# Optimization experiments

Hardware: AMD Instinct MI355X
Metric: run time of the kernel (lower is better)

The kernel has to match this reference:

```python
import jax, jax.numpy as jnp
import numpy as np

N_FFT = 512
HOP = N_FFT // 4  # torch.stft default hop_length
TWO_PI = 2.0 * np.pi


def _stft_phase(x):
    """torch.stft(x, n_fft=512, return_complex=True) phase: center reflect-pad,
    rectangular window, onesided rfft. Returns [F, T'] with F = n_fft//2+1."""
    pad = N_FFT // 2
    xp = jnp.pad(x, (pad, pad), mode='reflect')
    n_frames = (xp.shape[0] - N_FFT) // HOP + 1
    idx = (np.arange(n_frames, dtype=np.int32)[:, None] * HOP
           + np.arange(N_FFT, dtype=np.int32)[None, :])
    frames = xp[idx]                      # [T', n_fft]
    spec = jnp.fft.rfft(frames, axis=-1)  # [T', F]
    return jnp.angle(spec).T              # [F, T']


def _anti_wrap(x):
    return jnp.abs(x - jnp.round(x / TWO_PI) * TWO_PI)


def _gd(p):
    # banded matmul with gd_matrix == out[f] = p[f-1] - p[f], out[0] = -p[0]
    return jnp.concatenate([-p[:1], p[:-1] - p[1:]], axis=0)


def _iaf(p):
    # banded matmul with iaf_matrix along time axis
    return jnp.concatenate([-p[:, :1], p[:, :-1] - p[:, 1:]], axis=1)


def setup_inputs() -> dict:
    key = jax.random.key(0)
    k1, k2 = jax.random.split(key)
    T = 4194304  # 2^22 samples (~262 s @ 16 kHz)
    yd = jax.random.normal(k1, (T,), dtype=jnp.float32)
    td = jax.random.normal(k2, (T,), dtype=jnp.float32)
    return {"yd": yd, "td": td}


def reference(yd, td):
    pr = _stft_phase(yd)  # [F, T']
    pg = _stft_phase(td)
    ip_loss = jnp.mean(_anti_wrap(pr - pg))
    gd_loss = jnp.mean(_anti_wrap(_gd(pr) - _gd(pg)))
    iaf_loss = jnp.mean(_anti_wrap(_iaf(pr) - _iaf(pg)))
    return (ip_loss, gd_loss, iaf_loss)
```

## Files before the change

kernel.cpp:

```cpp
#include <hip/hip_runtime.h>
#include <math.h>

#define HOP     128
#define NSLOTS  256
#define FPW     8
#define PI_F    3.14159265358979323846f
#define PI2_F   1.57079632679489661923f
#define K8      0.70710678118654752440f

#define LDS_FENCE() do { __asm__ volatile("" ::: "memory"); \
                         __builtin_amdgcn_wave_barrier(); } while (0)

struct cpx { float x, y; };
__device__ __forceinline__ cpx cadd(cpx a, cpx b){ return {a.x+b.x, a.y+b.y}; }
__device__ __forceinline__ cpx csub(cpx a, cpx b){ return {a.x-b.x, a.y-b.y}; }
__device__ __forceinline__ cpx cmul(cpx a, cpx b){
    return {fmaf(a.x,b.x,-a.y*b.y), fmaf(a.x,b.y, a.y*b.x)};
}
__device__ __forceinline__ cpx cmulc(cpx a, cpx b){
    return {fmaf(a.x,b.x, a.y*b.y), fmaf(a.y,b.x,-a.x*b.y)};
}

__device__ __forceinline__ float abs_angle(float re, float im) {
    float a = fabsf(im), b = fabsf(re);
    float mn = fminf(a, b), mx = fmaxf(a, b);
    float t = __fdividef(mn, fmaxf(mx, 1e-37f));
    float t2 = t * t;
    float p = fmaf(t2, -0.0117212f, 0.05265332f);
    p = fmaf(t2, p, -0.11643287f);
    p = fmaf(t2, p, 0.19354346f);
    p = fmaf(t2, p, -0.33262347f);
    p = fmaf(t2, p, 0.99997726f);
    float r = t * p;
    r = (a > b) ? (PI2_F - r) : r;
    r = (re < 0.f) ? (PI_F - r) : r;
    return r;
}

__device__ __forceinline__ void dft8(cpx v[8]) {
    cpx a0=cadd(v[0],v[4]), a1=cadd(v[1],v[5]), a2=cadd(v[2],v[6]), a3=cadd(v[3],v[7]);
    cpx b0=csub(v[0],v[4]), b1=csub(v[1],v[5]), b2=csub(v[2],v[6]), b3=csub(v[3],v[7]);
    b1 = cpx{K8*(b1.x+b1.y), K8*(b1.y-b1.x)};
    b2 = cpx{b2.y, -b2.x};
    b3 = cpx{K8*(b3.y-b3.x), -K8*(b3.x+b3.y)};
    cpx c0=cadd(a0,a2), c2=csub(a0,a2);
    cpx c1=cadd(a1,a3), c3=csub(a1,a3); c3 = cpx{c3.y, -c3.x};
    cpx d0=cadd(b0,b2), d2=csub(b0,b2);
    cpx d1=cadd(b1,b3), d3=csub(b1,b3); d3 = cpx{d3.y, -d3.x};
    v[0]=cadd(c0,c1); v[4]=csub(c0,c1);
    v[2]=cadd(c2,c3); v[6]=csub(c2,c3);
    v[1]=cadd(d0,d1); v[5]=csub(d0,d1);
    v[3]=cadd(d2,d3); v[7]=csub(d2,d3);
}

__global__ __launch_bounds__(256, 2) void phase_loss_kernel(
        const float* __restrict__ y, const float* __restrict__ g,
        float* __restrict__ acc, int* __restrict__ ticket,
        float* __restrict__ out, int T, int n_frames, float inv_count) {
    __shared__ float2 xch_all[4][512];
    __shared__ float2 tw2_tab[7][8];
    __shared__ float wsum[3][4];
    __shared__ int is_last;

    const int tid  = threadIdx.x;
    const int lane = tid & 63;
    const int wid  = tid >> 6;
    const int l8   = lane & 7;
    float2* xch = xch_all[wid];

    if (tid < 56) {
        const int k = (tid >> 3) + 1, l = tid & 7;
        float s, c;
        __sincosf(-(2.0f * PI_F / 64.0f) * (float)(l * k), &s, &c);
        tw2_tab[tid >> 3][l] = make_float2(c, s);
    }
    __syncthreads();

    cpx tw1[7];
    #pragma unroll
    for (int k = 1; k < 8; ++k) {
        float a1 = -(2.0f * PI_F / 512.0f) * (float)(lane * k);
        __sincosf(a1, &tw1[k - 1].y, &tw1[k - 1].x);
    }

    float ip = 0.f, gd = 0.f, iaf = 0.f;
    cpx Cp[5];
    const int tmax_int = (T - 256) / HOP;
    const int ra1 = (lane >> 3) * 72 + (lane & 7);
    const int ra2 = (lane >> 3) * 65 + (lane & 7) * 8;
    const int rsl = (lane + 63) & 63;
    const int rsh = (64 - lane) & 63;

    auto load_frame = [&](int t, cpx* vv) {
        const int base = t * HOP - 256 + lane;
        if (t >= 2 && t <= tmax_int) {
            #pragma unroll
            for (int r = 0; r < 8; ++r) {
                int j = base + r * 64;
                vv[r].x = y[j]; vv[r].y = g[j];
            }
        } else {
            #pragma unroll
            for (int r = 0; r < 8; ++r) {
                int j = base + r * 64;
                j = (j < 0) ? -j : j;
                j = (j >= T) ? (2 * T - 2 - j) : j;
                vv[r].x = y[j]; vv[r].y = g[j];
            }
        }
    };

    auto process = [&](cpx* v, bool accum, bool hp) {
        dft8(v);
        #pragma unroll
        for (int k = 1; k < 8; ++k) v[k] = cmul(v[k], tw1[k - 1]);
        LDS_FENCE();
        #pragma unroll
        for (int k = 0; k < 8; ++k)
            xch[lane ^ (72 * k)] = make_float2(v[k].x, v[k].y);
        LDS_FENCE();
        #pragma unroll
        for (int r = 0; r < 8; ++r) {
            float2 tmp = xch[ra1 ^ (r << 3)];
            v[r] = cpx{tmp.x, tmp.y};
        }
        dft8(v);
        #pragma unroll
        for (int k = 1; k < 8; ++k) {
            float2 tw = tw2_tab[k - 1][l8];
            v[k] = cmul(v[k], cpx{tw.x, tw.y});
        }
        LDS_FENCE();
        #pragma unroll
        for (int k = 0; k < 8; ++k)
            xch[lane ^ (65 * k)] = make_float2(v[k].x, v[k].y);
        LDS_FENCE();
        #pragma unroll
        for (int r = 0; r < 8; ++r) {
            float2 tmp = xch[ra2 ^ r];
            v[r] = cpx{tmp.x, tmp.y};
        }
        dft8(v);
        cpx Cc[5];
        #pragma unroll
        for (int jj = 0; jj < 5; ++jj) {
            float px = __shfl(v[7 - jj].x, rsh, 64);
            float py = __shfl(v[7 - jj].y, rsh, 64);
            px = (lane == 0) ? v[(8 - jj) & 7].x : px;
            py = (lane == 0) ? v[(8 - jj) & 7].y : py;
            float ur = v[jj].x + px, ui = v[jj].y - py;
            float vx = v[jj].x - px, vy = v[jj].y + py;
            Cc[jj].x = fmaf(ur, vy, -ui * vx);
            Cc[jj].y = fmaf(ur, vx,  ui * vy);
        }
        if (accum) {
            cpx rprev = {0.f, 0.f};
            #pragma unroll
            for (int jj = 0; jj < 4; ++jj) {
                cpx rj;
                rj.x = __shfl(Cc[jj].x, rsl, 64);
                rj.y = __shfl(Cc[jj].y, rsl, 64);
                cpx cmj = (jj > 0 && lane == 0) ? rprev : rj;
                cpx cc = Cc[jj];
                float aw = abs_angle(cc.x, cc.y);
                ip += aw;
                cpx qg = cmulc(cmj, cc);
                float gt = abs_angle(qg.x, qg.y);
                gd += (jj == 0 && lane == 0) ? aw : gt;
                if (hp) {
                    cpx qi = cmulc(Cp[jj], cc);
                    iaf += abs_angle(qi.x, qi.y);
                } else {
                    iaf += aw;
                }
                rprev = rj;
            }
            if (lane == 0) {
                cpx cc = Cc[4];
                float aw = abs_angle(cc.x, cc.y);
                ip += aw;
                cpx qg = cmulc(rprev, cc);
                gd += abs_angle(qg.x, qg.y);
                if (hp) {
                    cpx qi = cmulc(Cp[4], cc);
                    iaf += abs_angle(qi.x, qi.y);
                } else {
                    iaf += aw;
                }
            }
        }
        #pragma unroll
        for (int jj = 0; jj < 5; ++jj) Cp[jj] = Cc[jj];
    };

    const int chain   = (blockIdx.x << 2) | wid;
    const int nchains = (int)(gridDim.x << 2);
    const int t0 = chain * FPW;
    int tend = t0 + FPW;
    if (chain == nchains - 1) tend = n_frames;
    const bool havep = (t0 > 0);

    cpx v[8];
    if (havep) {
        cpx vp[8];
        load_frame(t0 - 1, vp);
        load_frame(t0, v);
        process(vp, false, false);
    } else {
        load_frame(t0, v);
    }
    #pragma unroll 2
    for (int t = t0; t < tend; ++t) {
        cpx vn[8];
        const bool pf = (t + 1 < tend);
        if (pf) load_frame(t + 1, vn);
        process(v, true, havep || (t > t0));
        if (pf) {
            #pragma unroll
            for (int r = 0; r < 8; ++r) v[r] = vn[r];
        }
    }

    __syncthreads();
    for (int off = 32; off; off >>= 1) {
        ip  += __shfl_down(ip, off);
        gd  += __shfl_down(gd, off);
        iaf += __shfl_down(iaf, off);
    }
    if (lane == 0) { wsum[0][wid] = ip; wsum[1][wid] = gd; wsum[2][wid] = iaf; }
    __syncthreads();
    if (tid == 0) {
        const int slot = (int)(blockIdx.x & (NSLOTS - 1));
        atomicAdd(acc + 0 * NSLOTS + slot, wsum[0][0] + wsum[0][1] + wsum[0][2] + wsum[0][3]);
        atomicAdd(acc + 1 * NSLOTS + slot, wsum[1][0] + wsum[1][1] + wsum[1][2] + wsum[1][3]);
        atomicAdd(acc + 2 * NSLOTS + slot, wsum[2][0] + wsum[2][1] + wsum[2][2] + wsum[2][3]);
        __threadfence();
        is_last = (atomicAdd(ticket, 1) == (int)gridDim.x - 1);
    }
    __syncthreads();
    if (is_last) {
        for (int l = 0; l < 3; l++) {
            float vv = __hip_atomic_load(acc + l * NSLOTS + tid,
                                         __ATOMIC_RELAXED, __HIP_MEMORY_SCOPE_AGENT);
            for (int off = 32; off; off >>= 1) vv += __shfl_down(vv, off);
            if (lane == 0) wsum[l][wid] = vv;
        }
        __syncthreads();
        if (tid < 3)
            out[tid] = (wsum[tid][0] + wsum[tid][1] + wsum[tid][2] + wsum[tid][3]) * inv_count;
    }
}

extern "C" void kernel_launch(void* const* d_in, const int* in_sizes, int n_in,
                              void* d_out, int out_size, void* d_ws, size_t ws_size,
                              hipStream_t stream) {
    const float* y = (const float*)d_in[0];
    const float* g = (const float*)d_in[1];
    float* out = (float*)d_out;
    float* acc = (float*)d_ws;
    int* ticket = (int*)((char*)d_ws + 3 * NSLOTS * sizeof(float));
    const int T = in_sizes[0];
    const int n_frames = T / HOP + 1;
    int n_blocks = n_frames / (FPW * 4);
    if (n_blocks < 1) n_blocks = 1;

    hipMemsetAsync(d_ws, 0, 3 * NSLOTS * sizeof(float) + sizeof(int), stream);
    const float inv_count = 1.0f / (257.0f * (float)n_frames);
    phase_loss_kernel<<<n_blocks, 256, 0, stream>>>(y, g, acc, ticket, out,
                                                    T, n_frames, inv_count);
}
```

Measured before the change: 136.0 us.

## Process two interleaved frame chains per wavefront to raise instruction-level parallelism

Each wavefront now handles two independent chains of frames (A and B) at once. Their FFT stages, LDS exchanges and accumulation are interleaved, with a separate LDS exchange buffer per chain. The grid is halved to match, and the register-prefetch software pipeline of the next frame is dropped in favour of ILP across the two chains. This aims to hide LDS and shuffle latency, at the cost of higher register and LDS use, which may lower occupancy, and fewer blocks.

Measured after the change: 133.5 us. No clear change (-1.8%).

```diff
diff --git a/kernel.cpp b/kernel.cpp
--- a/kernel.cpp
+++ b/kernel.cpp
@@ -57,7 +57,7 @@
         const float* __restrict__ y, const float* __restrict__ g,
         float* __restrict__ acc, int* __restrict__ ticket,
         float* __restrict__ out, int T, int n_frames, float inv_count) {
-    __shared__ float2 xch_all[4][512];
+    __shared__ float2 xch_all[4][2][512];
     __shared__ float2 tw2_tab[7][8];
     __shared__ float wsum[3][4];
     __shared__ int is_last;
@@ -66,7 +66,8 @@
     const int lane = tid & 63;
     const int wid  = tid >> 6;
     const int l8   = lane & 7;
-    float2* xch = xch_all[wid];
+    float2* xcha = xch_all[wid][0];
+    float2* xchb = xch_all[wid][1];
 
     if (tid < 56) {
         const int k = (tid >> 3) + 1, l = tid & 7;
@@ -83,8 +84,12 @@
         __sincosf(a1, &tw1[k - 1].y, &tw1[k - 1].x);
     }
 
-    float ip = 0.f, gd = 0.f, iaf = 0.f;
-    cpx Cp[5];
+    float ipA = 0.f, gdA = 0.f, iafA = 0.f;
+    float ipB = 0.f, gdB = 0.f, iafB = 0.f;
+    cpx CpA[5], CpB[5];
+    #pragma unroll
+    for (int jj = 0; jj < 5; ++jj) { CpA[jj] = cpx{0.f,0.f}; CpB[jj] = cpx{0.f,0.f}; }
+
     const int tmax_int = (T - 256) / HOP;
     const int ra1 = (lane >> 3) * 72 + (lane & 7);
     const int ra2 = (lane >> 3) * 65 + (lane & 7) * 8;
@@ -110,38 +115,7 @@
         }
     };
 
-    auto process = [&](cpx* v, bool accum, bool hp) {
-        dft8(v);
-        #pragma unroll
-        for (int k = 1; k < 8; ++k) v[k] = cmul(v[k], tw1[k - 1]);
-        LDS_FENCE();
-        #pragma unroll
-        for (int k = 0; k < 8; ++k)
-            xch[lane ^ (72 * k)] = make_float2(v[k].x, v[k].y);
-        LDS_FENCE();
-        #pragma unroll
-        for (int r = 0; r < 8; ++r) {
-            float2 tmp = xch[ra1 ^ (r << 3)];
-            v[r] = cpx{tmp.x, tmp.y};
-        }
-        dft8(v);
-        #pragma unroll
-        for (int k = 1; k < 8; ++k) {
-            float2 tw = tw2_tab[k - 1][l8];
-            v[k] = cmul(v[k], cpx{tw.x, tw.y});
-        }
-        LDS_FENCE();
-        #pragma unroll
-        for (int k = 0; k < 8; ++k)
-            xch[lane ^ (65 * k)] = make_float2(v[k].x, v[k].y);
-        LDS_FENCE();
-        #pragma unroll
-        for (int r = 0; r < 8; ++r) {
-            float2 tmp = xch[ra2 ^ r];
-            v[r] = cpx{tmp.x, tmp.y};
-        }
-        dft8(v);
-        cpx Cc[5];
+    auto herm_C = [&](cpx* v, cpx* Cc) {
         #pragma unroll
         for (int jj = 0; jj < 5; ++jj) {
             float px = __shfl(v[7 - jj].x, rsh, 64);
@@ -153,73 +127,125 @@
             Cc[jj].x = fmaf(ur, vy, -ui * vx);
             Cc[jj].y = fmaf(ur, vx,  ui * vy);
         }
-        if (accum) {
-            cpx rprev = {0.f, 0.f};
-            #pragma unroll
-            for (int jj = 0; jj < 4; ++jj) {
-                cpx rj;
-                rj.x = __shfl(Cc[jj].x, rsl, 64);
-                rj.y = __shfl(Cc[jj].y, rsl, 64);
-                cpx cmj = (jj > 0 && lane == 0) ? rprev : rj;
-                cpx cc = Cc[jj];
-                float aw = abs_angle(cc.x, cc.y);
-                ip += aw;
-                cpx qg = cmulc(cmj, cc);
-                float gt = abs_angle(qg.x, qg.y);
-                gd += (jj == 0 && lane == 0) ? aw : gt;
-                if (hp) {
-                    cpx qi = cmulc(Cp[jj], cc);
-                    iaf += abs_angle(qi.x, qi.y);
-                } else {
-                    iaf += aw;
-                }
-                rprev = rj;
-            }
-            if (lane == 0) {
-                cpx cc = Cc[4];
-                float aw = abs_angle(cc.x, cc.y);
-                ip += aw;
-                cpx qg = cmulc(rprev, cc);
-                gd += abs_angle(qg.x, qg.y);
-                if (hp) {
-                    cpx qi = cmulc(Cp[4], cc);
-                    iaf += abs_angle(qi.x, qi.y);
-                } else {
-                    iaf += aw;
-                }
-            }
-        }
-        #pragma unroll
-        for (int jj = 0; jj < 5; ++jj) Cp[jj] = Cc[jj];
-    };
-
-    const int chain   = (blockIdx.x << 2) | wid;
-    const int nchains = (int)(gridDim.x << 2);
-    const int t0 = chain * FPW;
-    int tend = t0 + FPW;
-    if (chain == nchains - 1) tend = n_frames;
-    const bool havep = (t0 > 0);
-
-    cpx v[8];
-    if (havep) {
-        cpx vp[8];
-        load_frame(t0 - 1, vp);
-        load_frame(t0, v);
-        process(vp, false, false);
-    } else {
-        load_frame(t0, v);
-    }
-    #pragma unroll 2
-    for (int t = t0; t < tend; ++t) {
-        cpx vn[8];
-        const bool pf = (t + 1 < tend);
-        if (pf) load_frame(t + 1, vn);
-        process(v, true, havep || (t > t0));
-        if (pf) {
-            #pragma unroll
-            for (int r = 0; r < 8; ++r) v[r] = vn[r];
-        }
-    }
+    };
+
+    auto accum_frame = [&](cpx* Cc, cpx* Cp, float& ip, float& gd, float& iaf,
+                           bool hp) {
+        cpx rprev = {0.f, 0.f};
+        #pragma unroll
+        for (int jj = 0; jj < 4; ++jj) {
+            cpx rj;
+            rj.x = __shfl(Cc[jj].x, rsl, 64);
+            rj.y = __shfl(Cc[jj].y, rsl, 64);
+            cpx cmj = (jj > 0 && lane == 0) ? rprev : rj;
+            cpx cc = Cc[jj];
+            float aw = abs_angle(cc.x, cc.y);
+            ip += aw;
+            cpx qg = cmulc(cmj, cc);
+            float gt = abs_angle(qg.x, qg.y);
+            gd += (jj == 0 && lane == 0) ? aw : gt;
+            if (hp) {
+                cpx qi = cmulc(Cp[jj], cc);
+                iaf += abs_angle(qi.x, qi.y);
+            } else {
+                iaf += aw;
+            }
+            rprev = rj;
+        }
+        if (lane == 0) {
+            cpx cc = Cc[4];
+            float aw = abs_angle(cc.x, cc.y);
+            ip += aw;
+            cpx qg = cmulc(rprev, cc);
+            gd += abs_angle(qg.x, qg.y);
+            if (hp) {
+                cpx qi = cmulc(Cp[4], cc);
+                iaf += abs_angle(qi.x, qi.y);
+            } else {
+                iaf += aw;
+            }
+        }
+    };
+
+    auto process2 = [&](int tA, int tB, bool doA, bool doB, bool acc2,
+                        bool hpA, bool hpB) {
+        cpx va[8] = {}, vb[8] = {};
+        if (doA) load_frame(tA, va);
+        if (doB) load_frame(tB, vb);
+        dft8(va); dft8(vb);
+        #pragma unroll
+        for (int k = 1; k < 8; ++k) {
+            va[k] = cmul(va[k], tw1[k - 1]);
+            vb[k] = cmul(vb[k], tw1[k - 1]);
+        }
+        LDS_FENCE();
+        #pragma unroll
+        for (int k = 0; k < 8; ++k) {
+            xcha[lane ^ (72 * k)] = make_float2(va[k].x, va[k].y);
+            xchb[lane ^ (72 * k)] = make_float2(vb[k].x, vb[k].y);
+        }
+        LDS_FENCE();
+        #pragma unroll
+        for (int r = 0; r < 8; ++r) {
+            float2 ta = xcha[ra1 ^ (r << 3)];
+            float2 tb = xchb[ra1 ^ (r << 3)];
+            va[r] = cpx{ta.x, ta.y}; vb[r] = cpx{tb.x, tb.y};
+        }
+        dft8(va); dft8(vb);
+        #pragma unroll
+        for (int k = 1; k < 8; ++k) {
+            float2 tw = tw2_tab[k - 1][l8];
+            va[k] = cmul(va[k], cpx{tw.x, tw.y});
+            vb[k] = cmul(vb[k], cpx{tw.x, tw.y});
+        }
+        LDS_FENCE();
+        #pragma unroll
+        for (int k = 0; k < 8; ++k) {
+            xcha[lane ^ (65 * k)] = make_float2(va[k].x, va[k].y);
+            xchb[lane ^ (65 * k)] = make_float2(vb[k].x, vb[k].y);
+        }
+        LDS_FENCE();
+        #pragma unroll
+        for (int r = 0; r < 8; ++r) {
+            float2 ta = xcha[ra2 ^ r];
+            float2 tb = xchb[ra2 ^ r];
+            va[r] = cpx{ta.x, ta.y}; vb[r] = cpx{tb.x, tb.y};
+        }
+        dft8(va); dft8(vb);
+        cpx CcA[5], CcB[5];
+        herm_C(va, CcA);
+        herm_C(vb, CcB);
+        if (acc2) {
+            if (doA) accum_frame(CcA, CpA, ipA, gdA, iafA, hpA);
+            if (doB) accum_frame(CcB, CpB, ipB, gdB, iafB, hpB);
+        }
+        if (doA) {
+            #pragma unroll
+            for (int jj = 0; jj < 5; ++jj) CpA[jj] = CcA[jj];
+        }
+        if (doB) {
+            #pragma unroll
+            for (int jj = 0; jj < 5; ++jj) CpB[jj] = CcB[jj];
+        }
+    };
+
+    const int wch     = (blockIdx.x << 2) | wid;
+    const int nchains = (int)(gridDim.x << 3);
+    const int cA = wch * 2, cB = wch * 2 + 1;
+    const int t0A = cA * FPW, t0B = cB * FPW;
+    int tendB = t0B + FPW;
+    if (cB == nchains - 1) tendB = n_frames;
+    const bool havepA = (t0A > 0);
+
+    process2(t0A - 1, t0B - 1, havepA, true, false, false, false);
+    #pragma unroll 1
+    for (int t = 0; t < FPW; ++t)
+        process2(t0A + t, t0B + t, true, true, true, havepA || (t > 0), true);
+    #pragma unroll 1
+    for (int t = FPW; t < tendB - t0B; ++t)
+        process2(0, t0B + t, false, true, true, false, true);
+
+    float ip = ipA + ipB, gd = gdA + gdB, iaf = iafA + iafB;
 
     __syncthreads();
     for (int off = 32; off; off >>= 1) {
@@ -261,7 +287,7 @@
     int* ticket = (int*)((char*)d_ws + 3 * NSLOTS * sizeof(float));
     const int T = in_sizes[0];
     const int n_frames = T / HOP + 1;
-    int n_blocks = n_frames / (FPW * 4);
+    int n_blocks = n_frames / (FPW * 8);
     if (n_blocks < 1) n_blocks = 1;
 
     hipMemsetAsync(d_ws, 0, 3 * NSLOTS * sizeof(float) + sizeof(int), stream);
```
